# Kernel tuning notes

Measured on AMD Instinct MI355X. Metric: run time of the kernel, lower is better.

## Reference

```python
import jax, jax.numpy as jnp
import numpy as np

N_NODES = 50000
N_EDGES = 800000
H = 128   # hidden_dim
E = 64    # edge_dim
LN_EPS = 1e-5


def _layer_norm(x, g, b):
    m = jnp.mean(x, axis=-1, keepdims=True)
    v = jnp.mean(jnp.square(x - m), axis=-1, keepdims=True)
    return (x - m) * jax.lax.rsqrt(v + LN_EPS) * g + b


def _gelu(x):
    return jax.nn.gelu(x, approximate=False)  # torch default exact GELU


def setup_inputs() -> dict:
    key = jax.random.key(0)
    ks = jax.random.split(key, 24)

    def lin(k, fin, fout):
        kw, kb = jax.random.split(k)
        s = 1.0 / np.sqrt(fin)
        W = jax.random.uniform(kw, (fin, fout), jnp.float32, -s, s)
        b = jax.random.uniform(kb, (fout,), jnp.float32, -s, s)
        return W, b

    inp = {}
    inp["x"] = jax.random.normal(ks[0], (N_NODES, H), jnp.float32)
    inp["edge_emb"] = jax.random.normal(ks[1], (N_EDGES, E), jnp.float32)
    inp["time_weight"] = jax.random.uniform(ks[2], (N_EDGES, 1), jnp.float32)
    inp["message_node_scale"] = jax.random.uniform(ks[3], (N_NODES, 1), jnp.float32)
    inp["ln1_g"] = jnp.ones((H,), jnp.float32)
    inp["ln1_b"] = jnp.zeros((H,), jnp.float32)
    inp["ln2_g"] = jnp.ones((H,), jnp.float32)
    inp["ln2_b"] = jnp.zeros((H,), jnp.float32)
    inp["selfW"], inp["selfb"] = lin(ks[4], H, H)
    inp["msgW1"], inp["msgb1"] = lin(ks[5], H + E, H)
    inp["msgW2"], inp["msgb2"] = lin(ks[6], H, H)
    inp["gateW1"], inp["gateb1"] = lin(ks[7], 2 * H + E, H)
    inp["gateW2"], inp["gateb2"] = lin(ks[8], H, 1)
    inp["aggW"], inp["aggb"] = lin(ks[9], H, H)
    inp["ffnW1"], inp["ffnb1"] = lin(ks[10], H, 2 * H)
    inp["ffnW2"], inp["ffnb2"] = lin(ks[11], 2 * H, H)
    inp["edge_src"] = jax.random.randint(ks[12], (N_EDGES,), 0, N_NODES, jnp.int32)
    inp["edge_dst"] = jax.random.randint(ks[13], (N_EDGES,), 0, N_NODES, jnp.int32)
    return inp


def reference(x, edge_emb, time_weight, message_node_scale,
              ln1_g, ln1_b, ln2_g, ln2_b,
              selfW, selfb, msgW1, msgb1, msgW2, msgb2,
              gateW1, gateb1, gateW2, gateb2,
              aggW, aggb, ffnW1, ffnb1, ffnW2, ffnb2,
              edge_src, edge_dst):
    n_nodes = x.shape[0]
    n_edges = edge_dst.shape[0]

    h = _layer_norm(x, ln1_g, ln1_b)
    hs = h[edge_src]  # [NE, H]
    hd = h[edge_dst]  # [NE, H]

    msg = _gelu(jnp.concatenate([hs, edge_emb], -1) @ msgW1 + msgb1) @ msgW2 + msgb2
    gate = jax.nn.sigmoid(
        _gelu(jnp.concatenate([hd, hs, edge_emb], -1) @ gateW1 + gateb1) @ gateW2 + gateb2)
    edge_repr = gate * msg
    edge_repr = edge_repr * time_weight
    edge_scale = 0.5 * (message_node_scale[edge_src] + message_node_scale[edge_dst])
    edge_repr = edge_repr * edge_scale

    agg = jax.ops.segment_sum(edge_repr, edge_dst, num_segments=n_nodes)
    deg = jax.ops.segment_sum(jnp.ones((n_edges, 1), x.dtype), edge_dst,
                              num_segments=n_nodes)
    agg = agg / jnp.maximum(deg, 1.0)

    update = (h @ selfW + selfb) + (agg @ aggW + aggb)
    out = x + update  # residual; dropout is identity at inference

    h2 = _layer_norm(out, ln2_g, ln2_b)
    ffn_update = _gelu(h2 @ ffnW1 + ffnb1) @ ffnW2 + ffnb2
    out = out + ffn_update
    return (out, edge_repr)
```

## Files before the change

kernel.cpp:

```cpp
#include <hip/hip_runtime.h>


typedef __attribute__((ext_vector_type(8))) short short8;
typedef __attribute__((ext_vector_type(4))) float f32x4;

#define NN 50000
#define NEDGE 800000

#define MFMA(a, b, c) __builtin_amdgcn_mfma_f32_16x16x32_bf16(a, b, c, 0, 0, 0)

__device__ __forceinline__ unsigned short f2bf(float f) {
  unsigned int u = __float_as_uint(f);
  u += 0x7fffu + ((u >> 16) & 1u);
  return (unsigned short)(u >> 16);
}
__device__ __forceinline__ float bf2f(unsigned short u) {
  return __uint_as_float((unsigned int)u << 16);
}
__device__ __forceinline__ unsigned int cvtpk(float a, float b) {
  unsigned int d;
  asm("v_cvt_pk_bf16_f32 %0, %1, %2" : "=v"(d) : "v"(a), "v"(b));
  return d;
}
__device__ __forceinline__ unsigned short f2bf1(float a) {
  return (unsigned short)cvtpk(a, a);
}
__device__ __forceinline__ float geluf(float x) {
  const float t = x * fmaf(-0.1029437f, x * x, -2.3022211f);
  return x * __builtin_amdgcn_rcpf(1.0f + exp2f(t));
}
__device__ __forceinline__ short8 ld8(const unsigned short* p) {
  return *reinterpret_cast<const short8*>(p);
}
__device__ __forceinline__ int swz256(int row, int byteoff) {
  return row * 256 + (byteoff ^ ((row & 15) << 4));
}
__device__ __forceinline__ int swz128(int row, int byteoff) {
  return row * 128 + (byteoff ^ ((row & 7) << 4));
}

__device__ __forceinline__ void ln_frags(const float* __restrict__ rowp,
                                         const float* __restrict__ g,
                                         const float* __restrict__ b, int koff,
                                         short8 a[4]) {
  f32x4 v[8];
#pragma unroll
  for (int s = 0; s < 4; s++) {
    v[2 * s] = *reinterpret_cast<const f32x4*>(rowp + s * 32 + koff);
    v[2 * s + 1] = *reinterpret_cast<const f32x4*>(rowp + s * 32 + koff + 4);
  }
  float sm = 0.f;
#pragma unroll
  for (int i = 0; i < 8; i++) sm += v[i][0] + v[i][1] + v[i][2] + v[i][3];
  sm += __shfl_xor(sm, 16);
  sm += __shfl_xor(sm, 32);
  const float mean = sm * 0.0078125f;
  float sq = 0.f;
#pragma unroll
  for (int i = 0; i < 8; i++) {
#pragma unroll
    for (int t = 0; t < 4; t++) {
      const float d = v[i][t] - mean;
      sq += d * d;
    }
  }
  sq += __shfl_xor(sq, 16);
  sq += __shfl_xor(sq, 32);
  const float rs = rsqrtf(sq * 0.0078125f + 1e-5f);
#pragma unroll
  for (int s = 0; s < 4; s++) {
    const f32x4 glo = *reinterpret_cast<const f32x4*>(g + s * 32 + koff);
    const f32x4 ghi = *reinterpret_cast<const f32x4*>(g + s * 32 + koff + 4);
    const f32x4 blo = *reinterpret_cast<const f32x4*>(b + s * 32 + koff);
    const f32x4 bhi = *reinterpret_cast<const f32x4*>(b + s * 32 + koff + 4);
    float y[8];
#pragma unroll
    for (int t = 0; t < 4; t++) {
      y[t] = (v[2 * s][t] - mean) * rs * glo[t] + blo[t];
      y[4 + t] = (v[2 * s + 1][t] - mean) * rs * ghi[t] + bhi[t];
    }
    union { unsigned int u[4]; short8 s8; } pk;
    pk.u[0] = cvtpk(y[0], y[1]);
    pk.u[1] = cvtpk(y[2], y[3]);
    pk.u[2] = cvtpk(y[4], y[5]);
    pk.u[3] = cvtpk(y[6], y[7]);
    a[s] = pk.s8;
  }
}

__global__ __launch_bounds__(256) void prep_kernel(
    const float* __restrict__ selfW, const float* __restrict__ msgW1,
    const float* __restrict__ msgW2, const float* __restrict__ gateW1,
    const float* __restrict__ aggW, const float* __restrict__ ffnW1,
    const float* __restrict__ ffnW2, unsigned short* __restrict__ wts,
    int* __restrict__ cnt) {
  const int idx = blockIdx.x * 256 + threadIdx.x;
  if (idx <= NN) cnt[idx] = 0;
  if (idx < 16384) {
    int n = idx >> 7, k = idx & 127;
    wts[idx] = f2bf(selfW[k * 128 + n]);
  } else if (idx < 32768) {
    int l = idx - 16384, n = l >> 7, k = l & 127;
    wts[idx] = f2bf(aggW[k * 128 + n]);
  } else if (idx < 57344) {
    int l = idx - 32768, n = l / 192, k = l - n * 192;
    wts[idx] = f2bf(msgW1[k * 128 + n]);
  } else if (idx < 73728) {
    int l = idx - 57344, n = l >> 7, k = l & 127;
    wts[idx] = f2bf(msgW2[k * 128 + n]);
  } else if (idx < 114688) {
    int l = idx - 73728, n = l / 320, k = l - n * 320;
    wts[idx] = f2bf(gateW1[k * 128 + n]);
  } else if (idx < 147456) {
    int l = idx - 114688, n = l >> 7, k = l & 127;
    wts[idx] = f2bf(ffnW1[k * 256 + n]);
  } else if (idx < 180224) {
    int l = idx - 147456, n = l >> 8, k = l & 255;
    wts[idx] = f2bf(ffnW2[k * 128 + n]);
  }
}

__global__ __launch_bounds__(256) void node_pre_kernel(
    const float* __restrict__ x, const float* __restrict__ ln1g,
    const float* __restrict__ ln1b, const unsigned short* __restrict__ wts,
    unsigned short* __restrict__ pd, unsigned short* __restrict__ psm,
    float* __restrict__ aggf) {
  const int wid = threadIdx.x >> 6, lane = threadIdx.x & 63;
  const int q = lane >> 4, r16 = lane & 15, koff = q * 8;
  const int r0 = blockIdx.x * 64 + wid * 16;
  const int row = min(r0 + r16, NN - 1);
  {
    const int t = blockIdx.x * 256 + threadIdx.x;
    const f32x4 z = (f32x4){0.f, 0.f, 0.f, 0.f};
#pragma unroll
    for (int k = 0; k < 8; k++) {
      const int pos = t + k * 200192;
      if (pos < NN * 32) reinterpret_cast<f32x4*>(aggf)[pos] = z;
    }
  }
  const unsigned short* gateW1T = wts + 73728;
  const unsigned short* msgW1T = wts + 32768;
  short8 a[4];
  ln_frags(x + (size_t)row * 128, ln1g, ln1b, koff, a);
  f32x4 acc[3][8];
#pragma unroll
  for (int t = 0; t < 3; t++)
#pragma unroll
    for (int nt = 0; nt < 8; nt++) acc[t][nt] = (f32x4){0.f, 0.f, 0.f, 0.f};
#pragma unroll
  for (int s = 0; s < 4; s++) {
    const int k0 = s * 32 + koff;
#pragma unroll
    for (int nt = 0; nt < 8; nt++) {
      const int c = nt * 16 + r16;
      acc[0][nt] = MFMA(a[s], ld8(gateW1T + c * 320 + k0), acc[0][nt]);
      acc[1][nt] = MFMA(a[s], ld8(gateW1T + c * 320 + 128 + k0), acc[1][nt]);
      acc[2][nt] = MFMA(a[s], ld8(msgW1T + c * 192 + k0), acc[2][nt]);
    }
  }
#pragma unroll
  for (int j = 0; j < 4; j++) {
    const int gr = r0 + q * 4 + j;
    if (gr < NN) {
#pragma unroll
      for (int nt = 0; nt < 8; nt++) {
        const int c = nt * 16 + r16;
        pd[(size_t)gr * 128 + c] = f2bf(acc[0][nt][j]);
        psm[(size_t)gr * 256 + c] = f2bf(acc[1][nt][j]);
        psm[(size_t)gr * 256 + 128 + c] = f2bf(acc[2][nt][j]);
      }
    }
  }
}

__global__ __launch_bounds__(256) void count_kernel(
    const int* __restrict__ edst, int* __restrict__ cnt) {
  const int e = blockIdx.x * 256 + threadIdx.x;
  atomicAdd(&cnt[edst[e]], 1);
}

__global__ __launch_bounds__(256) void scan_sums_kernel(
    const int* __restrict__ cnt, int* __restrict__ bsum) {
  const int gi = blockIdx.x * 256 + threadIdx.x;
  int v = (gi < NN) ? cnt[gi] : 0;
#pragma unroll
  for (int m = 1; m < 64; m <<= 1) v += __shfl_xor(v, m);
  __shared__ int wsum[4];
  if ((threadIdx.x & 63) == 0) wsum[threadIdx.x >> 6] = v;
  __syncthreads();
  if (threadIdx.x == 0)
    bsum[blockIdx.x] = wsum[0] + wsum[1] + wsum[2] + wsum[3];
}

__global__ __launch_bounds__(256) void scan_final_kernel(
    const int* __restrict__ cnt, const int* __restrict__ bsum,
    int* __restrict__ row_start, int* __restrict__ cursor) {
  const int tid = threadIdx.x, lane = tid & 63, wid = tid >> 6;
  const int gi = blockIdx.x * 256 + tid;
  __shared__ int boff_s;
  __shared__ int wsum[4];
  if (wid == 0) {
    int pre = 0;
    for (int i = lane; i < blockIdx.x; i += 64) pre += bsum[i];
#pragma unroll
    for (int m = 32; m >= 1; m >>= 1) pre += __shfl_xor(pre, m);
    if (lane == 0) boff_s = pre;
  }
  const int val = (gi < NN) ? cnt[gi] : 0;
  int v = val;
#pragma unroll
  for (int d = 1; d < 64; d <<= 1) {
    const int t = __shfl_up(v, d);
    if (lane >= d) v += t;
  }
  if (lane == 63) wsum[wid] = v;
  __syncthreads();
  int woff = 0;
  for (int w = 0; w < wid; ++w) woff += wsum[w];
  const int excl = (v - val) + woff + boff_s;
  if (gi < NN) {
    row_start[gi] = excl;
    cursor[gi] = excl;
  }
  if (gi == NN - 1) row_start[NN] = excl + val;
}

__global__ __launch_bounds__(256) void scatter_kernel(
    const int* __restrict__ esrc, const int* __restrict__ edst,
    const float* __restrict__ tw, const float* __restrict__ mns,
    int* __restrict__ cursor, int4* __restrict__ etab) {
  const int e = blockIdx.x * 256 + threadIdx.x;
  const int si = esrc[e];
  const int di = edst[e];
  const int pos = atomicAdd(&cursor[di], 1);
  const float sc = tw[e] * 0.5f * (mns[si] + mns[di]);
  int4 v;
  v.x = e;
  v.y = si;
  v.z = di;
  v.w = __float_as_int(sc);
  etab[pos] = v;
}

__global__ __launch_bounds__(512, 6) void edge_kernel(
    const float* __restrict__ emb, const int4* __restrict__ etab,
    const unsigned short* __restrict__ pd,
    const unsigned short* __restrict__ psm,
    const unsigned short* __restrict__ wts, const float* __restrict__ msgb1,
    const float* __restrict__ msgb2, const float* __restrict__ gateb1,
    const float* __restrict__ gateW2, const float* __restrict__ gateb2v,
    float* __restrict__ erout, float* __restrict__ aggf) {
  __shared__ __align__(16) char buf[33792];
  __shared__ float p_s[4][64];
  __shared__ float G_s[64];
  __shared__ float sc_s[64];
  __shared__ int di_s[64], si_s[64], eidx_s[64];

  char* t1p = buf;
  char* embp = buf + 16384;
  float* xbuf = (float*)buf;

  const int tid = threadIdx.x;
  const int lane = tid & 63;
  const int wid = tid >> 6;
  const int q = lane >> 4;
  const int r16 = lane & 15;
  const int koff = q * 8;
  const int mg = wid >> 2;
  const int ng = wid & 3;
  const int e0 = blockIdx.x * 64;

  const unsigned short* gateW1T = wts + 73728;
  const unsigned short* msgW1T = wts + 32768;
  const unsigned short* msgW2T = wts + 57344;

  if (tid < 64) {
    const int4 et = etab[e0 + tid];
    eidx_s[tid] = et.x;
    si_s[tid] = et.y;
    di_s[tid] = et.z;
    sc_s[tid] = __int_as_float(et.w);
  }

#pragma unroll
  for (int r = 0; r < 2; r++) {
    const int unit = tid + 512 * r;
    const int row = unit >> 4;
    const int c4 = unit & 15;
    const int e = etab[e0 + row].x;
    const f32x4 v =
        *reinterpret_cast<const f32x4*>(emb + (size_t)e * 64 + c4 * 4);
    uint2 w;
    w.x = cvtpk(v[0], v[1]);
    w.y = cvtpk(v[2], v[3]);
    *reinterpret_cast<uint2*>(embp + swz128(row, c4 * 8)) = w;
  }
  __syncthreads();

  int cc[2];
  float g1[2], w2[2], b1m[2], b2m[2];
#pragma unroll
  for (int i = 0; i < 2; i++) {
    cc[i] = ng * 32 + i * 16 + r16;
    g1[i] = gateb1[cc[i]];
    w2[i] = gateW2[cc[i]];
    b1m[i] = msgb1[cc[i]];
    b2m[i] = msgb2[cc[i]];
  }

  short8 bI[2];
#pragma unroll
  for (int h = 0; h < 8; h++) {
    const int kk = koff + h;
    bI[0][h] = (kk == r16) ? (short)0x3F80 : (short)0;
    bI[1][h] = (kk == r16 + 16) ? (short)0x3F80 : (short)0;
  }

  f32x4 accg[2][2], acc1[2][2];
#pragma unroll
  for (int m = 0; m < 2; m++)
#pragma unroll
    for (int i = 0; i < 2; i++) {
      accg[m][i] = (f32x4){0.f, 0.f, 0.f, 0.f};
      acc1[m][i] = (f32x4){0.f, 0.f, 0.f, 0.f};
    }

  {
    const int kw = ng * 32 + koff;
#pragma unroll
    for (int m = 0; m < 2; m++) {
      const int row = mg * 32 + m * 16 + r16;
      const int si = si_s[row], di = di_s[row];
      const short8 apd = ld8(pd + (size_t)di * 128 + kw);
      const short8 aps = ld8(psm + (size_t)si * 256 + kw);
      const short8 apm = ld8(psm + (size_t)si * 256 + 128 + kw);
#pragma unroll
      for (int i = 0; i < 2; i++) {
        accg[m][i] = MFMA(apd, bI[i], accg[m][i]);
        accg[m][i] = MFMA(aps, bI[i], accg[m][i]);
        acc1[m][i] = MFMA(apm, bI[i], acc1[m][i]);
      }
    }
  }

#pragma unroll
  for (int s = 0; s < 2; s++) {
    const int k0 = s * 32 + koff;
    short8 a[2];
#pragma unroll
    for (int m = 0; m < 2; m++)
      a[m] = *reinterpret_cast<const short8*>(
          embp + swz128(mg * 32 + m * 16 + r16, k0 * 2));
#pragma unroll
    for (int i = 0; i < 2; i++) {
      const short8 bg = ld8(gateW1T + cc[i] * 320 + 256 + k0);
      const short8 bm = ld8(msgW1T + cc[i] * 192 + 128 + k0);
#pragma unroll
      for (int m = 0; m < 2; m++) {
        accg[m][i] = MFMA(a[m], bg, accg[m][i]);
        acc1[m][i] = MFMA(a[m], bm, acc1[m][i]);
      }
    }
  }

#pragma unroll
  for (int m = 0; m < 2; m++) {
#pragma unroll
    for (int j = 0; j < 4; j++) {
      const int row = mg * 32 + m * 16 + q * 4 + j;
      float v = geluf(accg[m][0][j] + g1[0]) * w2[0] +
                geluf(accg[m][1][j] + g1[1]) * w2[1];
      v += __shfl_xor(v, 1);
      v += __shfl_xor(v, 2);
      v += __shfl_xor(v, 4);
      v += __shfl_xor(v, 8);
      if (r16 == 0) p_s[ng][row] = v;
    }
  }

#pragma unroll
  for (int m = 0; m < 2; m++) {
#pragma unroll
    for (int i = 0; i < 2; i++) {
#pragma unroll
      for (int j = 0; j < 4; j++) {
        const int row = mg * 32 + m * 16 + q * 4 + j;
        *reinterpret_cast<unsigned short*>(t1p + swz256(row, cc[i] * 2)) =
            f2bf1(geluf(acc1[m][i][j] + b1m[i]));
      }
    }
  }
  __syncthreads();

  if (tid < 64) {
    const float p = gateb2v[0] + p_s[0][tid] + p_s[1][tid] + p_s[2][tid] +
                    p_s[3][tid];
    G_s[tid] =
        sc_s[tid] * __builtin_amdgcn_rcpf(1.f + exp2f(-1.4426950f * p));
  }

  f32x4 acc2[2][2];
#pragma unroll
  for (int m = 0; m < 2; m++)
#pragma unroll
    for (int i = 0; i < 2; i++) acc2[m][i] = (f32x4){0.f, 0.f, 0.f, 0.f};
#pragma unroll
  for (int s = 0; s < 4; s++) {
    const int k0 = s * 32 + koff;
    short8 a[2];
#pragma unroll
    for (int m = 0; m < 2; m++)
      a[m] = *reinterpret_cast<const short8*>(
          t1p + swz256(mg * 32 + m * 16 + r16, k0 * 2));
#pragma unroll
    for (int i = 0; i < 2; i++) {
      const short8 b = ld8(msgW2T + cc[i] * 128 + k0);
#pragma unroll
      for (int m = 0; m < 2; m++) acc2[m][i] = MFMA(a[m], b, acc2[m][i]);
    }
  }
  __syncthreads();

#pragma unroll
  for (int m = 0; m < 2; m++)
#pragma unroll
    for (int i = 0; i < 2; i++)
#pragma unroll
      for (int j = 0; j < 4; j++) {
        const int row = mg * 32 + m * 16 + q * 4 + j;
        xbuf[row * 132 + cc[i]] = G_s[row] * (acc2[m][i][j] + b2m[i]);
      }
  __syncthreads();

#pragma unroll
  for (int u = 0; u < 4; u++) {
    const int unit = tid + u * 512;
    const int r = unit >> 5;
    const int f4 = unit & 31;
    const f32x4 val = *reinterpret_cast<const f32x4*>(&xbuf[r * 132 + f4 * 4]);
    *reinterpret_cast<f32x4*>(erout + (size_t)eidx_s[r] * 128 + f4 * 4) = val;
  }

  {
    const int col = tid & 127;
    const int qt = tid >> 7;
    const int rbeg = qt * 16, rend = rbeg + 16;
    float acc = 0.f;
    int prev = di_s[rbeg];
    for (int r = rbeg; r < rend; ++r) {
      const int d = di_s[r];
      if (d != prev) {
        atomicAdd(&aggf[(size_t)prev * 128 + col], acc);
        acc = 0.f;
        prev = d;
      }
      acc += xbuf[r * 132 + col];
    }
    atomicAdd(&aggf[(size_t)prev * 128 + col], acc);
  }
}

__global__ __launch_bounds__(256) void node_ffn_kernel(
    const float* __restrict__ x, const float* __restrict__ ln1g,
    const float* __restrict__ ln1b, const float* __restrict__ aggf,
    const int* __restrict__ row_start, const unsigned short* __restrict__ wts,
    const float* __restrict__ selfb, const float* __restrict__ aggb,
    const float* __restrict__ ln2g, const float* __restrict__ ln2b,
    const float* __restrict__ fb1, const float* __restrict__ fb2,
    float* __restrict__ outp) {
  __shared__ unsigned short h2s[4][16 * 136];
  __shared__ unsigned short ts[4][16 * 264];
  const int wid = threadIdx.x >> 6, lane = threadIdx.x & 63;
  const int q = lane >> 4, r16 = lane & 15, koff = q * 8;
  const int r0 = blockIdx.x * 64 + wid * 16;
  const int row = min(r0 + r16, NN - 1);
  const float inv = __builtin_amdgcn_rcpf(
      fmaxf((float)(row_start[row + 1] - row_start[row]), 1.0f));
  const unsigned short* selfWT = wts;
  const unsigned short* aggWT = wts + 16384;
  const unsigned short* W1T = wts + 114688;
  const unsigned short* W2T = wts + 147456;

  short8 a1[4];
  ln_frags(x + (size_t)row * 128, ln1g, ln1b, koff, a1);
  f32x4 acc[8];
#pragma unroll
  for (int nt = 0; nt < 8; nt++) acc[nt] = (f32x4){0.f, 0.f, 0.f, 0.f};
#pragma unroll
  for (int s = 0; s < 4; s++) {
    const int k0 = s * 32 + koff;
    const float* ap = aggf + (size_t)row * 128 + k0;
    const f32x4 f0 = *reinterpret_cast<const f32x4*>(ap);
    const f32x4 f1 = *reinterpret_cast<const f32x4*>(ap + 4);
    union { unsigned int u[4]; short8 s; } pk;
    pk.u[0] = cvtpk(f0[0] * inv, f0[1] * inv);
    pk.u[1] = cvtpk(f0[2] * inv, f0[3] * inv);
    pk.u[2] = cvtpk(f1[0] * inv, f1[1] * inv);
    pk.u[3] = cvtpk(f1[2] * inv, f1[3] * inv);
#pragma unroll
    for (int nt = 0; nt < 8; nt++) {
      acc[nt] = MFMA(a1[s], ld8(selfWT + (nt * 16 + r16) * 128 + k0), acc[nt]);
      acc[nt] = MFMA(pk.s, ld8(aggWT + (nt * 16 + r16) * 128 + k0), acc[nt]);
    }
  }

  float o[8][4];
#pragma unroll
  for (int j = 0; j < 4; j++) {
    const int gr = min(r0 + q * 4 + j, NN - 1);
#pragma unroll
    for (int nt = 0; nt < 8; nt++) {
      const int c = r16 + 16 * nt;
      o[nt][j] = x[(size_t)gr * 128 + c] + acc[nt][j] + selfb[c] + aggb[c];
    }
  }

#pragma unroll
  for (int j = 0; j < 4; j++) {
    float s1 = 0.f;
#pragma unroll
    for (int nt = 0; nt < 8; nt++) s1 += o[nt][j];
    s1 += __shfl_xor(s1, 1);
    s1 += __shfl_xor(s1, 2);
    s1 += __shfl_xor(s1, 4);
    s1 += __shfl_xor(s1, 8);
    const float mean = s1 * 0.0078125f;
    float s2 = 0.f;
#pragma unroll
    for (int nt = 0; nt < 8; nt++) {
      const float d = o[nt][j] - mean;
      s2 += d * d;
    }
    s2 += __shfl_xor(s2, 1);
    s2 += __shfl_xor(s2, 2);
    s2 += __shfl_xor(s2, 4);
    s2 += __shfl_xor(s2, 8);
    const float rs = rsqrtf(s2 * 0.0078125f + 1e-5f);
#pragma unroll
    for (int nt = 0; nt < 8; nt++) {
      const int c = r16 + 16 * nt;
      h2s[wid][(q * 4 + j) * 136 + c] =
          f2bf1((o[nt][j] - mean) * rs * ln2g[c] + ln2b[c]);
    }
  }

  f32x4 acc1[16];
#pragma unroll
  for (int nt = 0; nt < 16; nt++) acc1[nt] = (f32x4){0.f, 0.f, 0.f, 0.f};
#pragma unroll
  for (int s = 0; s < 4; s++) {
    const int k0 = s * 32 + koff;
    const short8 a =
        *reinterpret_cast<const short8*>(&h2s[wid][r16 * 136 + k0]);
#pragma unroll
    for (int nt = 0; nt < 16; nt++)
      acc1[nt] = MFMA(a, ld8(W1T + (nt * 16 + r16) * 128 + k0), acc1[nt]);
  }
#pragma unroll
  for (int nt = 0; nt < 16; nt++) {
    const int c = r16 + 16 * nt;
    const float bb = fb1[c];
#pragma unroll
    for (int j = 0; j < 4; j++)
      ts[wid][(q * 4 + j) * 264 + c] = f2bf1(geluf(acc1[nt][j] + bb));
  }

  f32x4 acc2[8];
#pragma unroll
  for (int nt = 0; nt < 8; nt++) acc2[nt] = (f32x4){0.f, 0.f, 0.f, 0.f};
#pragma unroll
  for (int s = 0; s < 8; s++) {
    const int k0 = s * 32 + koff;
    const short8 av =
        *reinterpret_cast<const short8*>(&ts[wid][r16 * 264 + k0]);
#pragma unroll
    for (int nt = 0; nt < 8; nt++)
      acc2[nt] = MFMA(av, ld8(W2T + (nt * 16 + r16) * 256 + k0), acc2[nt]);
  }

#pragma unroll
  for (int j = 0; j < 4; j++) {
    const int gr = r0 + q * 4 + j;
    if (gr < NN) {
#pragma unroll
      for (int nt = 0; nt < 8; nt++) {
        const int c = r16 + 16 * nt;
        outp[(size_t)gr * 128 + c] = o[nt][j] + acc2[nt][j] + fb2[c];
      }
    }
  }
}

extern "C" void kernel_launch(void* const* d_in, const int* in_sizes, int n_in,
                              void* d_out, int out_size, void* d_ws,
                              size_t ws_size, hipStream_t stream) {
  (void)in_sizes; (void)n_in; (void)out_size; (void)ws_size;
  const float* x = (const float*)d_in[0];
  const float* emb = (const float*)d_in[1];
  const float* tw = (const float*)d_in[2];
  const float* mns = (const float*)d_in[3];
  const float* ln1g = (const float*)d_in[4];
  const float* ln1b = (const float*)d_in[5];
  const float* ln2g = (const float*)d_in[6];
  const float* ln2b = (const float*)d_in[7];
  const float* selfW = (const float*)d_in[8];
  const float* selfb = (const float*)d_in[9];
  const float* msgW1 = (const float*)d_in[10];
  const float* msgb1 = (const float*)d_in[11];
  const float* msgW2 = (const float*)d_in[12];
  const float* msgb2 = (const float*)d_in[13];
  const float* gateW1 = (const float*)d_in[14];
  const float* gateb1 = (const float*)d_in[15];
  const float* gateW2 = (const float*)d_in[16];
  const float* gateb2 = (const float*)d_in[17];
  const float* aggW = (const float*)d_in[18];
  const float* aggb = (const float*)d_in[19];
  const float* ffnW1 = (const float*)d_in[20];
  const float* ffnb1 = (const float*)d_in[21];
  const float* ffnW2 = (const float*)d_in[22];
  const float* ffnb2 = (const float*)d_in[23];
  const int* esrc = (const int*)d_in[24];
  const int* edst = (const int*)d_in[25];

  char* ws = (char*)d_ws;
  unsigned short* pdb = (unsigned short*)(ws);
  unsigned short* psmb = (unsigned short*)(ws + 25600000);
  unsigned short* wts = (unsigned short*)(ws + 76800000);
  int* cnt = (int*)(ws + 77160448);
  int* row_start = (int*)(ws + 77360640);
  int* cursor = (int*)(ws + 77560832);
  int* bsum = (int*)(ws + 77761024);
  int4* etab = (int4*)(ws + 77763072);

  float* out_nodes = (float*)d_out;
  float* out_edges = out_nodes + (size_t)NN * 128;
  float* aggf = out_nodes;

  const int NB_SCAN = (NN + 255) / 256;

  prep_kernel<<<704, 256, 0, stream>>>(selfW, msgW1, msgW2, gateW1, aggW,
                                       ffnW1, ffnW2, wts, cnt);
  node_pre_kernel<<<782, 256, 0, stream>>>(x, ln1g, ln1b, wts, pdb, psmb,
                                           aggf);
  count_kernel<<<3125, 256, 0, stream>>>(edst, cnt);
  scan_sums_kernel<<<NB_SCAN, 256, 0, stream>>>(cnt, bsum);
  scan_final_kernel<<<NB_SCAN, 256, 0, stream>>>(cnt, bsum, row_start, cursor);
  scatter_kernel<<<3125, 256, 0, stream>>>(esrc, edst, tw, mns, cursor, etab);
  edge_kernel<<<12500, 512, 0, stream>>>(emb, etab, pdb, psmb, wts, msgb1,
                                         msgb2, gateb1, gateW2, gateb2,
                                         out_edges, aggf);
  node_ffn_kernel<<<782, 256, 0, stream>>>(x, ln1g, ln1b, aggf, row_start,
                                           wts, selfb, aggb, ln2g, ln2b,
                                           ffnb1, ffnb2, out_nodes);
}
```

Baseline: 616.6 us.

## Stage gathered node projections in LDS and fold degree count into node_pre

The edge kernel now gathers each edge's destination and source node projections cooperatively into shared memory with full-row coalesced loads, pre-summing the two gate contributions in fp32 before packing to bf16, so one identity MFMA replaces two. The t1 buffer reuses the message staging area. Separately, the per-edge degree-count atomics move into node_pre_kernel, removing one kernel launch. LDS per block grows from about 33KB to 40KB, which may reduce occupancy, and the pre-sum adds an extra bf16 rounding step.

```diff
diff --git a/kernel.cpp b/kernel.cpp
--- a/kernel.cpp
+++ b/kernel.cpp
@@ -123,8 +123,9 @@
 __global__ __launch_bounds__(256) void node_pre_kernel(
     const float* __restrict__ x, const float* __restrict__ ln1g,
     const float* __restrict__ ln1b, const unsigned short* __restrict__ wts,
-    unsigned short* __restrict__ pd, unsigned short* __restrict__ psm,
-    float* __restrict__ aggf) {
+    const int* __restrict__ edst, unsigned short* __restrict__ pd,
+    unsigned short* __restrict__ psm, float* __restrict__ aggf,
+    int* __restrict__ cnt) {
   const int wid = threadIdx.x >> 6, lane = threadIdx.x & 63;
   const int q = lane >> 4, r16 = lane & 15, koff = q * 8;
   const int r0 = blockIdx.x * 64 + wid * 16;
@@ -137,6 +138,11 @@
       const int pos = t + k * 200192;
       if (pos < NN * 32) reinterpret_cast<f32x4*>(aggf)[pos] = z;
     }
+#pragma unroll
+    for (int k = 0; k < 4; k++) {
+      const int e = t + k * 200192;
+      if (e < NEDGE) atomicAdd(&cnt[edst[e]], 1);
+    }
   }
   const unsigned short* gateW1T = wts + 73728;
   const unsigned short* msgW1T = wts + 32768;
@@ -171,12 +177,6 @@
       }
     }
   }
-}
-
-__global__ __launch_bounds__(256) void count_kernel(
-    const int* __restrict__ edst, int* __restrict__ cnt) {
-  const int e = blockIdx.x * 256 + threadIdx.x;
-  atomicAdd(&cnt[edst[e]], 1);
 }
 
 __global__ __launch_bounds__(256) void scan_sums_kernel(
@@ -250,14 +250,15 @@
     const float* __restrict__ msgb2, const float* __restrict__ gateb1,
     const float* __restrict__ gateW2, const float* __restrict__ gateb2v,
     float* __restrict__ erout, float* __restrict__ aggf) {
-  __shared__ __align__(16) char buf[33792];
+  __shared__ __align__(16) char buf[64 * 256 + 64 * 256 + 64 * 128];
   __shared__ float p_s[4][64];
   __shared__ float G_s[64];
   __shared__ float sc_s[64];
-  __shared__ int di_s[64], si_s[64], eidx_s[64];
-
-  char* t1p = buf;
-  char* embp = buf + 16384;
+  __shared__ int di_s[64], eidx_s[64];
+
+  char* pgp = buf;
+  char* pmp = buf + 16384;
+  char* embp = buf + 32768;
   float* xbuf = (float*)buf;
 
   const int tid = threadIdx.x;
@@ -277,11 +278,32 @@
   if (tid < 64) {
     const int4 et = etab[e0 + tid];
     eidx_s[tid] = et.x;
-    si_s[tid] = et.y;
     di_s[tid] = et.z;
     sc_s[tid] = __int_as_float(et.w);
   }
 
+#pragma unroll
+  for (int r = 0; r < 2; r++) {
+    const int unit = tid + 512 * r;
+    const int row = unit >> 4;
+    const int c = unit & 15;
+    const int4 et = etab[e0 + row];
+    const int si = et.y, di = et.z;
+    const short8 vd = ld8(pd + (size_t)di * 128 + c * 8);
+    const short8 vs = ld8(psm + (size_t)si * 256 + c * 8);
+    union { unsigned int u[4]; short8 s; } pk;
+#pragma unroll
+    for (int h = 0; h < 4; h++) {
+      const float f0 =
+          bf2f((unsigned short)vd[2 * h]) + bf2f((unsigned short)vs[2 * h]);
+      const float f1 = bf2f((unsigned short)vd[2 * h + 1]) +
+                       bf2f((unsigned short)vs[2 * h + 1]);
+      pk.u[h] = cvtpk(f0, f1);
+    }
+    *reinterpret_cast<short8*>(pgp + swz256(row, c * 16)) = pk.s;
+    *reinterpret_cast<short8*>(pmp + swz256(row, c * 16)) =
+        ld8(psm + (size_t)si * 256 + 128 + c * 8);
+  }
 #pragma unroll
   for (int r = 0; r < 2; r++) {
     const int unit = tid + 512 * r;
@@ -330,14 +352,13 @@
 #pragma unroll
     for (int m = 0; m < 2; m++) {
       const int row = mg * 32 + m * 16 + r16;
-      const int si = si_s[row], di = di_s[row];
-      const short8 apd = ld8(pd + (size_t)di * 128 + kw);
-      const short8 aps = ld8(psm + (size_t)si * 256 + kw);
-      const short8 apm = ld8(psm + (size_t)si * 256 + 128 + kw);
+      const short8 apg =
+          *reinterpret_cast<const short8*>(pgp + swz256(row, kw * 2));
+      const short8 apm =
+          *reinterpret_cast<const short8*>(pmp + swz256(row, kw * 2));
 #pragma unroll
       for (int i = 0; i < 2; i++) {
-        accg[m][i] = MFMA(apd, bI[i], accg[m][i]);
-        accg[m][i] = MFMA(aps, bI[i], accg[m][i]);
+        accg[m][i] = MFMA(apg, bI[i], accg[m][i]);
         acc1[m][i] = MFMA(apm, bI[i], acc1[m][i]);
       }
     }
@@ -385,7 +406,7 @@
 #pragma unroll
       for (int j = 0; j < 4; j++) {
         const int row = mg * 32 + m * 16 + q * 4 + j;
-        *reinterpret_cast<unsigned short*>(t1p + swz256(row, cc[i] * 2)) =
+        *reinterpret_cast<unsigned short*>(pmp + swz256(row, cc[i] * 2)) =
             f2bf1(geluf(acc1[m][i][j] + b1m[i]));
       }
     }
@@ -411,7 +432,7 @@
 #pragma unroll
     for (int m = 0; m < 2; m++)
       a[m] = *reinterpret_cast<const short8*>(
-          t1p + swz256(mg * 32 + m * 16 + r16, k0 * 2));
+          pmp + swz256(mg * 32 + m * 16 + r16, k0 * 2));
 #pragma unroll
     for (int i = 0; i < 2; i++) {
       const short8 b = ld8(msgW2T + cc[i] * 128 + k0);
@@ -640,9 +661,8 @@
 
   prep_kernel<<<704, 256, 0, stream>>>(selfW, msgW1, msgW2, gateW1, aggW,
                                        ffnW1, ffnW2, wts, cnt);
-  node_pre_kernel<<<782, 256, 0, stream>>>(x, ln1g, ln1b, wts, pdb, psmb,
-                                           aggf);
-  count_kernel<<<3125, 256, 0, stream>>>(edst, cnt);
+  node_pre_kernel<<<782, 256, 0, stream>>>(x, ln1g, ln1b, wts, edst, pdb,
+                                           psmb, aggf, cnt);
   scan_sums_kernel<<<NB_SCAN, 256, 0, stream>>>(cnt, bsum);
   scan_final_kernel<<<NB_SCAN, 256, 0, stream>>>(cnt, bsum, row_start, cursor);
   scatter_kernel<<<3125, 256, 0, stream>>>(esrc, edst, tw, mns, cursor, etab);
```

Result: faster. 582.5 us (median of 2 runs) (-5.5%).
